# Kernel optimization log

Hardware: AMD Instinct MI355X
Metric: run time of the kernel (lower is better)

Reference implementation:

```python
import jax, jax.numpy as jnp
import numpy as np

N = 20000      # num_nodes
E = 320000     # num_edges
T = 24         # seq_len
SD = 16        # static_dim
DD = 8         # dynamic_dim
HID = 128      # hidden_dim
HEADS = 4
DPH = HID // HEADS  # per-head dim (GATConv out_channels = hidden_dim // heads)
L = 3          # num_gnn_layers
LN_EPS = 1e-5


def setup_inputs() -> dict:
    key = jax.random.key(0)
    ks = jax.random.split(key, 16)
    f = lambda i, shape, s=0.1: jax.random.normal(ks[i], shape, jnp.float32) * s
    return {
        "x_static": f(0, (N, SD), 1.0),
        "x_dynamic": f(1, (T, N, DD), 1.0),
        "edge_index": jax.random.randint(ks[2], (2, E), 0, N),
        "proj_W": f(3, (SD + DD, HID)),
        "proj_b": jnp.zeros((HID,), jnp.float32),
        "gat_W": f(4, (L, HID, HID)),
        "att_src": f(5, (L, HEADS, DPH)),
        "att_dst": f(6, (L, HEADS, DPH)),
        "gat_b": jnp.zeros((L, HID), jnp.float32),
        "ln_g": jnp.ones((L, HID), jnp.float32),
        "ln_b": jnp.zeros((L, HID), jnp.float32),
        "lstm_Wih0": f(7, (4 * HID, HID)),
        "lstm_Whh0": f(8, (4 * HID, HID)),
        "lstm_bih0": jnp.zeros((4 * HID,), jnp.float32),
        "lstm_bhh0": jnp.zeros((4 * HID,), jnp.float32),
        "lstm_Wih1": f(9, (4 * HID, HID)),
        "lstm_Whh1": f(10, (4 * HID, HID)),
        "lstm_bih1": jnp.zeros((4 * HID,), jnp.float32),
        "lstm_bhh1": jnp.zeros((4 * HID,), jnp.float32),
        "out_W1": f(11, (HID, HID // 2)),
        "out_b1": jnp.zeros((HID // 2,), jnp.float32),
        "out_W2": f(12, (HID // 2, 1)),
        "out_b2": jnp.zeros((1,), jnp.float32),
    }


def _gat_layer(h, src, dst, W, a_s, a_d, b, g, beta):
    """PyG GATConv (self-loops already in src/dst) + residual + LayerNorm + ReLU."""
    Nn = h.shape[0]
    xp = (h @ W).reshape(Nn, HEADS, DPH)                # [N, H, D]
    a_src = (xp * a_s).sum(-1)                          # [N, H]
    a_dst = (xp * a_d).sum(-1)                          # [N, H]
    e = jax.nn.leaky_relu(a_src[src] + a_dst[dst], 0.2)  # [E', H]
    m = jax.ops.segment_max(e, dst, num_segments=Nn)
    ex = jnp.exp(e - m[dst])
    denom = jax.ops.segment_sum(ex, dst, num_segments=Nn)
    alpha = ex / (denom[dst] + 1e-16)                   # segment softmax over in-edges
    msg = xp[src] * alpha[:, :, None]                   # [E', H, D]
    out = jax.ops.segment_sum(msg, dst, num_segments=Nn).reshape(Nn, HID) + b
    out = out + h                                       # residual (dims match)
    mu = out.mean(-1, keepdims=True)
    var = ((out - mu) ** 2).mean(-1, keepdims=True)
    out = g * (out - mu) * jax.lax.rsqrt(var + LN_EPS) + beta
    return jax.nn.relu(out)


def _lstm_cell(x, h, c, Wih, Whh, bih, bhh):
    z = x @ Wih.T + h @ Whh.T + bih + bhh
    i, f, gg, o = jnp.split(z, 4, axis=-1)              # torch gate order i,f,g,o
    c = jax.nn.sigmoid(f) * c + jax.nn.sigmoid(i) * jnp.tanh(gg)
    h = jax.nn.sigmoid(o) * jnp.tanh(c)
    return h, c


def reference(x_static, x_dynamic, edge_index, proj_W, proj_b, gat_W, att_src,
              att_dst, gat_b, ln_g, ln_b, lstm_Wih0, lstm_Whh0, lstm_bih0,
              lstm_bhh0, lstm_Wih1, lstm_Whh1, lstm_bih1, lstm_bhh1,
              out_W1, out_b1, out_W2, out_b2):
    Nn = x_static.shape[0]
    loop = jnp.arange(Nn)
    src = jnp.concatenate([edge_index[0], loop])        # GATConv add_self_loops=True
    dst = jnp.concatenate([edge_index[1], loop])

    @jax.checkpoint
    def timestep(xd_t):
        h = jnp.concatenate([x_static, xd_t], axis=-1) @ proj_W + proj_b
        for l in range(L):
            h = _gat_layer(h, src, dst, gat_W[l], att_src[l], att_dst[l],
                           gat_b[l], ln_g[l], ln_b[l])
        return h

    h_seq = jax.lax.map(timestep, x_dynamic)            # [T, N, HID]

    def step(carry, x_t):
        h0, c0, h1, c1 = carry
        h0, c0 = _lstm_cell(x_t, h0, c0, lstm_Wih0, lstm_Whh0, lstm_bih0, lstm_bhh0)
        h1, c1 = _lstm_cell(h0, h1, c1, lstm_Wih1, lstm_Whh1, lstm_bih1, lstm_bhh1)
        return (h0, c0, h1, c1), None

    z = jnp.zeros((Nn, HID), x_static.dtype)
    (_, _, h1, _), _ = jax.lax.scan(step, (z, z, z, z), h_seq)
    pred = jax.nn.relu(h1 @ out_W1 + out_b1) @ out_W2 + out_b2
    return pred[:, 0]
```

## Files before the change

kernel.cpp:

```cpp
#include <hip/hip_runtime.h>
#include <hip/hip_bf16.h>
#include <math.h>

#define NN   20000
#define NE   320000
#define TT   24
#define SDIM 16
#define DDIM 8
#define HID  128
#define HEADS 4
#define DPH  32
#define NL   3
#define TC   4

typedef unsigned short u16;
typedef unsigned int   u32;
typedef __attribute__((ext_vector_type(8))) short  short8;
typedef __attribute__((ext_vector_type(4))) float  floatx4;

__device__ __forceinline__ u16 f2bf(float x) {
  u32 u = __float_as_uint(x);
  return (u16)((u + 0x7fff + ((u >> 16) & 1)) >> 16);
}
__device__ __forceinline__ float bf2f(u16 b) {
  return __uint_as_float(((u32)b) << 16);
}

__global__ void k_count(const int* __restrict__ dst, int* __restrict__ cnt) {
  int e = blockIdx.x * 256 + threadIdx.x;
  if (e < NE) atomicAdd(&cnt[dst[e]], 1);
}

__global__ __launch_bounds__(1024) void k_scan(const int* __restrict__ cnt,
    int* __restrict__ rowptr, int* __restrict__ cursor) {
  __shared__ int sh[1024];
  int tid = threadIdx.x;
  const int CH = 20;
  int base = tid * CH;
  int local[CH];
  int s = 0;
  #pragma unroll
  for (int i = 0; i < CH; i++) {
    int idx = base + i;
    int v = (idx < NN) ? cnt[idx] : 0;
    local[i] = s;
    s += v;
  }
  sh[tid] = s;
  __syncthreads();
  for (int off = 1; off < 1024; off <<= 1) {
    int tv = (tid >= off) ? sh[tid - off] : 0;
    __syncthreads();
    sh[tid] += tv;
    __syncthreads();
  }
  int pre = (tid > 0) ? sh[tid - 1] : 0;
  #pragma unroll
  for (int i = 0; i < CH; i++) {
    int idx = base + i;
    if (idx < NN) { int e = pre + local[i]; rowptr[idx] = e; cursor[idx] = e; }
  }
  if (tid == 1023) rowptr[NN] = sh[1023];
}

__global__ void k_fill(const int* __restrict__ src, const int* __restrict__ dst,
    int* __restrict__ cursor, int* __restrict__ col, int* __restrict__ row) {
  int e = blockIdx.x * 256 + threadIdx.x;
  if (e < NE) {
    int d = dst[e];
    int pos = atomicAdd(&cursor[d], 1);
    col[pos] = src[e];
    row[pos] = d;
  }
}

__global__ void k_prepw_lstm(const float* __restrict__ Wih, const float* __restrict__ Whh,
    u16* __restrict__ Bt) {
  int idx = blockIdx.x * 256 + threadIdx.x;
  if (idx < 512 * 256) {
    int jp = idx >> 8, k = idx & 255;
    int c = jp >> 2, g = jp & 3;
    int j = g * 128 + c;
    float v = (k < 128) ? Wih[(size_t)j * 128 + k] : Whh[(size_t)j * 128 + (k - 128)];
    Bt[idx] = f2bf(v);
  }
}
__global__ void k_prepb(const float* __restrict__ bih0, const float* __restrict__ bhh0,
    const float* __restrict__ bih1, const float* __restrict__ bhh1,
    float* __restrict__ bs01) {
  int t = threadIdx.x;
  const float* bih = blockIdx.x ? bih1 : bih0;
  const float* bhh = blockIdx.x ? bhh1 : bhh0;
  int c = t >> 2, g = t & 3;
  bs01[blockIdx.x * 512 + t] = bih[g * 128 + c] + bhh[g * 128 + c];
}
__global__ void k_prepw_gat(const float* __restrict__ gatW, u16* __restrict__ Btg) {
  int idx = blockIdx.x * 256 + threadIdx.x;
  if (idx < NL * 128 * 128) {
    int l = idx >> 14, r = idx & 16383;
    int n = r >> 7, k = r & 127;
    Btg[idx] = f2bf(gatW[(size_t)l * 16384 + k * 128 + n]);
  }
}

__global__ __launch_bounds__(256) void k_proj(const float* __restrict__ xs,
    const float* __restrict__ xdt, const float* __restrict__ W,
    const float* __restrict__ b, u16* __restrict__ hbf) {
  __shared__ float Ws[24 * HID];
  __shared__ float xin[16][24];
  int tid = threadIdx.x;
  int tc = blockIdx.y;
  for (int i = tid; i < 24 * HID; i += 256) Ws[i] = W[i];
  int n0 = blockIdx.x * 16;
  for (int i = tid; i < 16 * 24; i += 256) {
    int r = i / 24, c = i % 24;
    int n = n0 + r;
    xin[r][c] = (c < SDIM) ? xs[(size_t)n * SDIM + c]
                           : xdt[(size_t)tc * NN * DDIM + (size_t)n * DDIM + (c - SDIM)];
  }
  __syncthreads();
  int ch = tid & 127, rb = (tid >> 7) * 8;
  for (int r = rb; r < rb + 8; r++) {
    float acc = b[ch];
    #pragma unroll
    for (int k = 0; k < 24; k++) acc = fmaf(xin[r][k], Ws[k * HID + ch], acc);
    hbf[((size_t)tc * NN + n0 + r) * HID + ch] = f2bf(acc);
  }
}

#define TBM 128
#define TBN 64
#define TBK 64

__global__ __launch_bounds__(256) void k_bgemm_gat(const u16* __restrict__ A,
    const u16* __restrict__ Bt, const float* __restrict__ as_,
    const float* __restrict__ ad_, u16* __restrict__ xpbf,
    float* __restrict__ asrc, float* __restrict__ adst, int M) {
  __shared__ u16 As[TBM][TBK + 8];
  __shared__ u16 Bs[TBN][TBK + 8];
  int tid = threadIdx.x;
  int wid = tid >> 6, lane = tid & 63;
  int wr = wid >> 1, wc = wid & 1;
  int lrow = lane & 15, lgrp = lane >> 4;
  int row0 = blockIdx.x * TBM, col0 = blockIdx.y * TBN;
  floatx4 acc[4][2] = {};
  for (int k0 = 0; k0 < 128; k0 += TBK) {
    #pragma unroll
    for (int i = 0; i < 4; i++) {
      int idx = tid + i * 256;
      int r = idx >> 3, g = idx & 7;
      int gr = row0 + r;
      short8 v = {};
      if (gr < M) v = *(const short8*)(A + (size_t)gr * 128 + k0 + g * 8);
      *(short8*)&As[r][g * 8] = v;
    }
    #pragma unroll
    for (int i = 0; i < 2; i++) {
      int idx = tid + i * 256;
      int r = idx >> 3, g = idx & 7;
      *(short8*)&Bs[r][g * 8] = *(const short8*)(Bt + (size_t)(col0 + r) * 128 + k0 + g * 8);
    }
    __syncthreads();
    #pragma unroll
    for (int kk = 0; kk < TBK; kk += 32) {
      short8 bfr[2];
      #pragma unroll
      for (int n = 0; n < 2; n++)
        bfr[n] = *(const short8*)&Bs[wc * 32 + n * 16 + lrow][kk + lgrp * 8];
      #pragma unroll
      for (int m = 0; m < 4; m++) {
        short8 af = *(const short8*)&As[wr * 64 + m * 16 + lrow][kk + lgrp * 8];
        acc[m][0] = __builtin_amdgcn_mfma_f32_16x16x32_bf16(af, bfr[0], acc[m][0], 0, 0, 0);
        acc[m][1] = __builtin_amdgcn_mfma_f32_16x16x32_bf16(af, bfr[1], acc[m][1], 0, 0, 0);
      }
    }
    __syncthreads();
  }
  int head = (col0 >> 5) + wc;
  float as0 = as_[head * 32 + lrow], as1 = as_[head * 32 + 16 + lrow];
  float ad0 = ad_[head * 32 + lrow], ad1 = ad_[head * 32 + 16 + lrow];
  #pragma unroll
  for (int m = 0; m < 4; m++) {
    #pragma unroll
    for (int r = 0; r < 4; r++) {
      int grow = row0 + wr * 64 + m * 16 + lgrp * 4 + r;
      float v0 = acc[m][0][r], v1 = acc[m][1][r];
      if (grow < M) {
        xpbf[(size_t)grow * HID + col0 + wc * 32 + lrow]      = f2bf(v0);
        xpbf[(size_t)grow * HID + col0 + wc * 32 + 16 + lrow] = f2bf(v1);
      }
      float ps = v0 * as0 + v1 * as1;
      float pd = v0 * ad0 + v1 * ad1;
      #pragma unroll
      for (int off = 1; off < 16; off <<= 1) {
        ps += __shfl_xor(ps, off);
        pd += __shfl_xor(pd, off);
      }
      if (lrow == 0 && grow < M) {
        asrc[grow * HEADS + head] = ps;
        adst[grow * HEADS + head] = pd;
      }
    }
  }
}

__global__ __launch_bounds__(256) void k_edgew(const int* __restrict__ col,
    const int* __restrict__ row, const float* __restrict__ asrc,
    const float* __restrict__ adst, float* __restrict__ wbuf) {
  int idx = blockIdx.x * 256 + threadIdx.x;
  int h = idx & 3;
  int je = idx >> 2;
  int tc = je / NE;
  int j = je - tc * NE;
  int base = tc * NN;
  float ev = asrc[(size_t)(base + col[j]) * HEADS + h]
           + adst[(size_t)(base + row[j]) * HEADS + h];
  ev = (ev > 0.f) ? ev : 0.2f * ev;
  wbuf[idx] = __expf(fminf(ev, 80.f));
}

__global__ __launch_bounds__(256) void k_aggr(const u16* __restrict__ xpbf,
    u16* __restrict__ hbf, const float* __restrict__ asrc,
    const float* __restrict__ adst, const float* __restrict__ wbuf,
    const int* __restrict__ rowptr, const int* __restrict__ col,
    const float* __restrict__ bias, const float* __restrict__ lng,
    const float* __restrict__ lnb) {
  int wid = threadIdx.x >> 6, lane = threadIdx.x & 63;
  int n = blockIdx.x * 4 + wid;
  int tc = n / NN;
  int node = n - tc * NN, base = tc * NN;
  int hh = lane >> 4;
  float ad = adst[n * HEADS + hh];
  float e0 = asrc[n * HEADS + hh] + ad;
  e0 = (e0 > 0.f) ? e0 : 0.2f * e0;
  float w0 = __expf(fminf(e0, 80.f));
  u32 xv = ((const u32*)(xpbf + (size_t)n * HID))[lane];
  float den0 = w0, den1 = 0.f, den2 = 0.f, den3 = 0.f;
  float p00 = w0 * bf2f((u16)(xv & 0xffff)), p10 = 0.f, p20 = 0.f, p30 = 0.f;
  float p01 = w0 * bf2f((u16)(xv >> 16)),    p11 = 0.f, p21 = 0.f, p31 = 0.f;
  const float* wrow = wbuf + (size_t)tc * NE * HEADS;
  int rs = rowptr[node], re = rowptr[node + 1];
  int j = rs;
  for (; j + 4 <= re; j += 4) {
    float w0e = wrow[(size_t)(j + 0) * HEADS + hh];
    float w1e = wrow[(size_t)(j + 1) * HEADS + hh];
    float w2e = wrow[(size_t)(j + 2) * HEADS + hh];
    float w3e = wrow[(size_t)(j + 3) * HEADS + hh];
    int s0 = base + col[j],     s1 = base + col[j + 1];
    int s2 = base + col[j + 2], s3 = base + col[j + 3];
    u32 x0 = ((const u32*)(xpbf + (size_t)s0 * HID))[lane];
    u32 x1 = ((const u32*)(xpbf + (size_t)s1 * HID))[lane];
    u32 x2 = ((const u32*)(xpbf + (size_t)s2 * HID))[lane];
    u32 x3 = ((const u32*)(xpbf + (size_t)s3 * HID))[lane];
    den0 += w0e; den1 += w1e; den2 += w2e; den3 += w3e;
    p00 = fmaf(w0e, bf2f((u16)(x0 & 0xffff)), p00);
    p10 = fmaf(w1e, bf2f((u16)(x1 & 0xffff)), p10);
    p20 = fmaf(w2e, bf2f((u16)(x2 & 0xffff)), p20);
    p30 = fmaf(w3e, bf2f((u16)(x3 & 0xffff)), p30);
    p01 = fmaf(w0e, bf2f((u16)(x0 >> 16)), p01);
    p11 = fmaf(w1e, bf2f((u16)(x1 >> 16)), p11);
    p21 = fmaf(w2e, bf2f((u16)(x2 >> 16)), p21);
    p31 = fmaf(w3e, bf2f((u16)(x3 >> 16)), p31);
  }
  for (; j < re; j++) {
    float w = wrow[(size_t)j * HEADS + hh];
    int s0 = base + col[j];
    u32 x0 = ((const u32*)(xpbf + (size_t)s0 * HID))[lane];
    den0 += w;
    p00 = fmaf(w, bf2f((u16)(x0 & 0xffff)), p00);
    p01 = fmaf(w, bf2f((u16)(x0 >> 16)), p01);
  }
  float den = (den0 + den1) + (den2 + den3);
  float mg0 = (p00 + p10) + (p20 + p30);
  float mg1 = (p01 + p11) + (p21 + p31);
  float inv = 1.f / (den + 1e-16f);
  int c0 = lane * 2;
  size_t hoff = (size_t)n * HID + c0;
  u32 hv = *(const u32*)(hbf + hoff);
  float o0 = mg0 * inv + bias[c0]     + bf2f((u16)(hv & 0xffff));
  float o1 = mg1 * inv + bias[c0 + 1] + bf2f((u16)(hv >> 16));
  float s2 = o0 + o1;
  #pragma unroll
  for (int off = 32; off; off >>= 1) s2 += __shfl_xor(s2, off);
  float mu = s2 * (1.f / HID);
  float d0 = o0 - mu, d1 = o1 - mu;
  float v2 = d0 * d0 + d1 * d1;
  #pragma unroll
  for (int off = 32; off; off >>= 1) v2 += __shfl_xor(v2, off);
  float rstd = rsqrtf(v2 * (1.f / HID) + 1e-5f);
  o0 = lng[c0] * d0 * rstd + lnb[c0];
  o1 = lng[c0 + 1] * d1 * rstd + lnb[c0 + 1];
  o0 = fmaxf(o0, 0.f);
  o1 = fmaxf(o1, 0.f);
  *(u32*)(hbf + hoff) = (u32)f2bf(o0) | ((u32)f2bf(o1) << 16);
}

__device__ __forceinline__ void lstm_body(const u16* __restrict__ A0,
    const u16* __restrict__ A1, const u16* __restrict__ Bt,
    const float* __restrict__ bs, float* __restrict__ cst,
    u16* __restrict__ hout, char* smem, int bx, int by) {
  u16 (*As)[TBK + 8] = (u16(*)[TBK + 8])smem;
  u16 (*Bs)[TBK + 8] = (u16(*)[TBK + 8])(smem + TBM * (TBK + 8) * 2);
  float (*zs)[68] = (float(*)[68])smem;
  int tid = threadIdx.x;
  int wid = tid >> 6, lane = tid & 63;
  int wr = wid >> 1, wc = wid & 1;
  int lrow = lane & 15, lgrp = lane >> 4;
  int row0 = bx * TBM, col0 = by * TBN;
  floatx4 acc[4][2] = {};
  for (int k0 = 0; k0 < 256; k0 += TBK) {
    const u16* Ap = (k0 < 128) ? A0 : A1;
    int kb = k0 & 127;
    #pragma unroll
    for (int i = 0; i < 4; i++) {
      int idx = tid + i * 256;
      int r = idx >> 3, g = idx & 7;
      int gr = row0 + r;
      short8 v = {};
      if (gr < NN) v = *(const short8*)(Ap + (size_t)gr * 128 + kb + g * 8);
      *(short8*)&As[r][g * 8] = v;
    }
    #pragma unroll
    for (int i = 0; i < 2; i++) {
      int idx = tid + i * 256;
      int r = idx >> 3, g = idx & 7;
      *(short8*)&Bs[r][g * 8] = *(const short8*)(Bt + (size_t)(col0 + r) * 256 + k0 + g * 8);
    }
    __syncthreads();
    #pragma unroll
    for (int kk = 0; kk < TBK; kk += 32) {
      short8 bfr[2];
      #pragma unroll
      for (int n = 0; n < 2; n++)
        bfr[n] = *(const short8*)&Bs[wc * 32 + n * 16 + lrow][kk + lgrp * 8];
      #pragma unroll
      for (int m = 0; m < 4; m++) {
        short8 af = *(const short8*)&As[wr * 64 + m * 16 + lrow][kk + lgrp * 8];
        acc[m][0] = __builtin_amdgcn_mfma_f32_16x16x32_bf16(af, bfr[0], acc[m][0], 0, 0, 0);
        acc[m][1] = __builtin_amdgcn_mfma_f32_16x16x32_bf16(af, bfr[1], acc[m][1], 0, 0, 0);
      }
    }
    __syncthreads();
  }
  #pragma unroll
  for (int m = 0; m < 4; m++)
    #pragma unroll
    for (int n = 0; n < 2; n++)
      #pragma unroll
      for (int r = 0; r < 4; r++)
        zs[wr * 64 + m * 16 + lgrp * 4 + r][wc * 32 + n * 16 + lrow] = acc[m][n][r];
  __syncthreads();
  int ch0 = by * 16;
  #pragma unroll
  for (int it = 0; it < 8; it++) {
    int o = tid + it * 256;
    int r = o >> 4, lc = o & 15;
    int grow = row0 + r;
    if (grow < NN) {
      float4 zi = *(float4*)&zs[r][lc * 4];
      int ch = ch0 + lc;
      size_t gi = (size_t)grow * HID + ch;
      float ii = zi.x + bs[4 * ch + 0];
      float ff = zi.y + bs[4 * ch + 1];
      float gg = zi.z + bs[4 * ch + 2];
      float oo = zi.w + bs[4 * ch + 3];
      float si = 1.f / (1.f + __expf(-ii));
      float sf = 1.f / (1.f + __expf(-ff));
      float so = 1.f / (1.f + __expf(-oo));
      float tg = tanhf(gg);
      float cn = sf * cst[gi] + si * tg;
      cst[gi] = cn;
      hout[gi] = f2bf(so * tanhf(cn));
    }
  }
}

__global__ __launch_bounds__(256) void k_lstm1(const u16* __restrict__ A0,
    const u16* __restrict__ A1, const u16* __restrict__ Bt,
    const float* __restrict__ bs, float* __restrict__ cst, u16* __restrict__ hout) {
  __shared__ __align__(16) char smem[34816];
  lstm_body(A0, A1, Bt, bs, cst, hout, smem, blockIdx.x, blockIdx.y);
}

__global__ __launch_bounds__(256) void k_lstm2(
    const u16* __restrict__ A0a, const u16* __restrict__ A1a, const u16* __restrict__ Bta,
    const float* __restrict__ bsa, float* __restrict__ csta, u16* __restrict__ houta,
    const u16* __restrict__ A0b, const u16* __restrict__ A1b, const u16* __restrict__ Btb,
    const float* __restrict__ bsb, float* __restrict__ cstb, u16* __restrict__ houtb) {
  __shared__ __align__(16) char smem[34816];
  if (blockIdx.z == 0) lstm_body(A0a, A1a, Bta, bsa, csta, houta, smem, blockIdx.x, blockIdx.y);
  else                 lstm_body(A0b, A1b, Btb, bsb, cstb, houtb, smem, blockIdx.x, blockIdx.y);
}

__global__ __launch_bounds__(64) void k_mlp(const u16* __restrict__ h1,
    const float* __restrict__ W1, const float* __restrict__ b1,
    const float* __restrict__ W2, const float* __restrict__ b2,
    float* __restrict__ out) {
  int n = blockIdx.x, j = threadIdx.x;
  const u16* hr = h1 + (size_t)n * HID;
  float acc = b1[j];
  #pragma unroll 8
  for (int k = 0; k < HID; k++) acc = fmaf(bf2f(hr[k]), W1[(size_t)k * 64 + j], acc);
  acc = fmaxf(acc, 0.f);
  float p = acc * W2[j];
  #pragma unroll
  for (int off = 32; off; off >>= 1) p += __shfl_xor(p, off);
  if (j == 0) out[n] = p + b2[0];
}

extern "C" void kernel_launch(void* const* d_in, const int* in_sizes, int n_in,
                              void* d_out, int out_size, void* d_ws, size_t ws_size,
                              hipStream_t stream) {
  const float* xs    = (const float*)d_in[0];
  const float* xd    = (const float*)d_in[1];
  const int*   ei    = (const int*)d_in[2];
  const float* projW = (const float*)d_in[3];
  const float* projb = (const float*)d_in[4];
  const float* gatW  = (const float*)d_in[5];
  const float* attS  = (const float*)d_in[6];
  const float* attD  = (const float*)d_in[7];
  const float* gatb  = (const float*)d_in[8];
  const float* lng   = (const float*)d_in[9];
  const float* lnb   = (const float*)d_in[10];
  const float* Wih0  = (const float*)d_in[11];
  const float* Whh0  = (const float*)d_in[12];
  const float* bih0  = (const float*)d_in[13];
  const float* bhh0  = (const float*)d_in[14];
  const float* Wih1  = (const float*)d_in[15];
  const float* Whh1  = (const float*)d_in[16];
  const float* bih1  = (const float*)d_in[17];
  const float* bhh1  = (const float*)d_in[18];
  const float* oW1   = (const float*)d_in[19];
  const float* ob1   = (const float*)d_in[20];
  const float* oW2   = (const float*)d_in[21];
  const float* ob2   = (const float*)d_in[22];
  float* out = (float*)d_out;

  char* w = (char*)d_ws;
  size_t off = 0;
  auto alloc = [&](size_t bytes) { void* p = w + off; off += (bytes + 255) & ~(size_t)255; return p; };
  u16*   hbf   = (u16*)  alloc((size_t)TC * NN * HID * 2);
  u16*   xpbf  = (u16*)  alloc((size_t)TC * NN * HID * 2);
  float* asrc  = (float*)alloc((size_t)TC * NN * HEADS * 4);
  float* adst  = (float*)alloc((size_t)TC * NN * HEADS * 4);
  float* wbuf  = (float*)alloc((size_t)TC * NE * HEADS * 4);
  float* c01   = (float*)alloc((size_t)2 * NN * HID * 4);
  float* c0 = c01, *c1 = c01 + (size_t)NN * HID;
  u16*   h0p   = (u16*)  alloc((size_t)2 * NN * HID * 2);
  u16*   h1p   = (u16*)  alloc((size_t)2 * NN * HID * 2);
  u16*   h0buf[2] = { h0p, h0p + (size_t)NN * HID };
  u16*   h1buf[2] = { h1p, h1p + (size_t)NN * HID };
  u16*   Wc0bf = (u16*)alloc((size_t)512 * 256 * 2);
  u16*   Wc1bf = (u16*)alloc((size_t)512 * 256 * 2);
  float* bs01  = (float*)alloc((size_t)1024 * 4);
  float* bs0 = bs01, *bs1 = bs01 + 512;
  u16*   gatWbf= (u16*)alloc((size_t)NL * 128 * 128 * 2);
  int* cnt    = (int*)alloc((size_t)NN * 4);
  int* rowptr = (int*)alloc((size_t)(NN + 1) * 4);
  int* cursor = (int*)alloc((size_t)NN * 4);
  int* col    = (int*)alloc((size_t)NE * 4);
  int* rowi   = (int*)alloc((size_t)NE * 4);

  const int* esrc = ei;
  const int* edst = ei + NE;

  hipMemsetAsync(cnt, 0, (size_t)NN * 4, stream);
  k_count<<<(NE + 255) / 256, 256, 0, stream>>>(edst, cnt);
  k_scan<<<1, 1024, 0, stream>>>(cnt, rowptr, cursor);
  k_fill<<<(NE + 255) / 256, 256, 0, stream>>>(esrc, edst, cursor, col, rowi);

  k_prepw_lstm<<<(512 * 256) / 256, 256, 0, stream>>>(Wih0, Whh0, Wc0bf);
  k_prepw_lstm<<<(512 * 256) / 256, 256, 0, stream>>>(Wih1, Whh1, Wc1bf);
  k_prepb<<<2, 512, 0, stream>>>(bih0, bhh0, bih1, bhh1, bs01);
  k_prepw_gat<<<(NL * 128 * 128) / 256, 256, 0, stream>>>(gatW, gatWbf);
  hipMemsetAsync(c01, 0, (size_t)2 * NN * HID * 4, stream);
  hipMemsetAsync(h0buf[0], 0, (size_t)NN * HID * 2, stream);
  hipMemsetAsync(h1buf[0], 0, (size_t)NN * HID * 2, stream);

  const int gx  = (NN + TBM - 1) / TBM;
  const int gx2 = (TC * NN + TBM - 1) / TBM;

  auto gnn_chunk = [&](int tcb) {
    k_proj<<<dim3(NN / 16, TC), 256, 0, stream>>>(
        xs, xd + (size_t)(tcb * TC) * NN * DDIM, projW, projb, hbf);
    for (int l = 0; l < NL; l++) {
      k_bgemm_gat<<<dim3(gx2, 2), 256, 0, stream>>>(
          hbf, gatWbf + (size_t)l * 128 * 128,
          attS + l * HEADS * DPH, attD + l * HEADS * DPH,
          xpbf, asrc, adst, TC * NN);
      k_edgew<<<(TC * NE * HEADS) / 256, 256, 0, stream>>>(col, rowi, asrc, adst, wbuf);
      k_aggr<<<TC * NN / 4, 256, 0, stream>>>(
          xpbf, hbf, asrc, adst, wbuf, rowptr, col, gatb + (size_t)l * HID,
          lng + (size_t)l * HID, lnb + (size_t)l * HID);
    }
  };
  auto lstm_merged = [&](int t) {
    int pi = t & 1;
    int s1 = (t + 1) & (TC - 1);
    k_lstm2<<<dim3(gx, 8, 2), 256, 0, stream>>>(
        h0buf[pi ^ 1], h1buf[pi], Wc1bf, bs1, c1, h1buf[pi ^ 1],
        hbf + (size_t)s1 * NN * HID, h0buf[pi ^ 1], Wc0bf, bs0, c0, h0buf[pi]);
  };

  gnn_chunk(0);
  k_lstm1<<<dim3(gx, 8), 256, 0, stream>>>(hbf, h0buf[0], Wc0bf, bs0, c0, h0buf[1]);
  lstm_merged(0); lstm_merged(1); lstm_merged(2);
  for (int tcb = 1; tcb < TT / TC; tcb++) {
    gnn_chunk(tcb);
    lstm_merged(4 * tcb - 1);
    lstm_merged(4 * tcb);
    lstm_merged(4 * tcb + 1);
    if (tcb < TT / TC - 1) lstm_merged(4 * tcb + 2);
    else {
      lstm_merged(4 * tcb + 2);
      k_lstm1<<<dim3(gx, 8), 256, 0, stream>>>(h0buf[0], h1buf[1], Wc1bf, bs1, c1, h1buf[0]);
    }
  }

  k_mlp<<<NN, 64, 0, stream>>>(h1buf[0], oW1, ob1, oW2, ob2, out);
}
```

Before: 3.318 ms.

## Batch timestep chunk per edge in GAT aggregation and drop LDS staging in LSTM epilogue

The edge-weight kernel now computes all four timesteps of a chunk per edge and packs them as bf16 into one 64-bit word. The aggregation kernel handles one node across all four timesteps, so each edge's column index and weights are loaded once and shared across the 16 lanes of a head by shuffles. This cuts index and weight traffic and shrinks the weight buffer, at the cost of bf16 precision on attention weights and more registers per thread. The LSTM epilogue now regroups the MFMA accumulators with lane shuffles instead of an LDS round trip and a barrier, which also shrinks shared memory.

```diff
diff --git a/kernel.cpp b/kernel.cpp
--- a/kernel.cpp
+++ b/kernel.cpp
@@ -15,6 +15,7 @@
 
 typedef unsigned short u16;
 typedef unsigned int   u32;
+typedef unsigned long long u64;
 typedef __attribute__((ext_vector_type(8))) short  short8;
 typedef __attribute__((ext_vector_type(4))) float  floatx4;
 
@@ -206,93 +207,93 @@
 
 __global__ __launch_bounds__(256) void k_edgew(const int* __restrict__ col,
     const int* __restrict__ row, const float* __restrict__ asrc,
-    const float* __restrict__ adst, float* __restrict__ wbuf) {
+    const float* __restrict__ adst, u64* __restrict__ ewq) {
   int idx = blockIdx.x * 256 + threadIdx.x;
-  int h = idx & 3;
-  int je = idx >> 2;
-  int tc = je / NE;
-  int j = je - tc * NE;
-  int base = tc * NN;
-  float ev = asrc[(size_t)(base + col[j]) * HEADS + h]
-           + adst[(size_t)(base + row[j]) * HEADS + h];
-  ev = (ev > 0.f) ? ev : 0.2f * ev;
-  wbuf[idx] = __expf(fminf(ev, 80.f));
+  int j = idx >> 2, h = idx & 3;
+  int c = col[j], r = row[j];
+  u64 w = 0;
+  #pragma unroll
+  for (int tc = 0; tc < TC; tc++) {
+    float ev = asrc[((size_t)tc * NN + c) * HEADS + h]
+             + adst[((size_t)tc * NN + r) * HEADS + h];
+    ev = (ev > 0.f) ? ev : 0.2f * ev;
+    w |= ((u64)f2bf(__expf(fminf(ev, 80.f)))) << (tc * 16);
+  }
+  ewq[idx] = w;
 }
 
 __global__ __launch_bounds__(256) void k_aggr(const u16* __restrict__ xpbf,
     u16* __restrict__ hbf, const float* __restrict__ asrc,
-    const float* __restrict__ adst, const float* __restrict__ wbuf,
+    const float* __restrict__ adst, const u64* __restrict__ ewq,
     const int* __restrict__ rowptr, const int* __restrict__ col,
     const float* __restrict__ bias, const float* __restrict__ lng,
     const float* __restrict__ lnb) {
   int wid = threadIdx.x >> 6, lane = threadIdx.x & 63;
-  int n = blockIdx.x * 4 + wid;
-  int tc = n / NN;
-  int node = n - tc * NN, base = tc * NN;
-  int hh = lane >> 4;
-  float ad = adst[n * HEADS + hh];
-  float e0 = asrc[n * HEADS + hh] + ad;
-  e0 = (e0 > 0.f) ? e0 : 0.2f * e0;
-  float w0 = __expf(fminf(e0, 80.f));
-  u32 xv = ((const u32*)(xpbf + (size_t)n * HID))[lane];
-  float den0 = w0, den1 = 0.f, den2 = 0.f, den3 = 0.f;
-  float p00 = w0 * bf2f((u16)(xv & 0xffff)), p10 = 0.f, p20 = 0.f, p30 = 0.f;
-  float p01 = w0 * bf2f((u16)(xv >> 16)),    p11 = 0.f, p21 = 0.f, p31 = 0.f;
-  const float* wrow = wbuf + (size_t)tc * NE * HEADS;
+  int node = blockIdx.x * 4 + wid;
+  int hh = lane >> 4, lrow = lane & 15;
+  int c0 = lane * 2;
+  float bi0 = bias[c0], bi1 = bias[c0 + 1];
+  float g0 = lng[c0], g1 = lng[c0 + 1];
+  float lb0 = lnb[c0], lb1 = lnb[c0 + 1];
+  float den[TC], p0[TC], p1[TC];
+  u32 hv[TC];
+  #pragma unroll
+  for (int tc = 0; tc < TC; tc++) {
+    size_t n = (size_t)tc * NN + node;
+    float ad = adst[n * HEADS + hh];
+    float e0 = asrc[n * HEADS + hh] + ad;
+    e0 = (e0 > 0.f) ? e0 : 0.2f * e0;
+    float w0 = __expf(fminf(e0, 80.f));
+    u32 xv = ((const u32*)(xpbf + n * HID))[lane];
+    den[tc] = w0;
+    p0[tc] = w0 * bf2f((u16)(xv & 0xffff));
+    p1[tc] = w0 * bf2f((u16)(xv >> 16));
+    hv[tc] = *(const u32*)(hbf + n * HID + c0);
+  }
   int rs = rowptr[node], re = rowptr[node + 1];
-  int j = rs;
-  for (; j + 4 <= re; j += 4) {
-    float w0e = wrow[(size_t)(j + 0) * HEADS + hh];
-    float w1e = wrow[(size_t)(j + 1) * HEADS + hh];
-    float w2e = wrow[(size_t)(j + 2) * HEADS + hh];
-    float w3e = wrow[(size_t)(j + 3) * HEADS + hh];
-    int s0 = base + col[j],     s1 = base + col[j + 1];
-    int s2 = base + col[j + 2], s3 = base + col[j + 3];
-    u32 x0 = ((const u32*)(xpbf + (size_t)s0 * HID))[lane];
-    u32 x1 = ((const u32*)(xpbf + (size_t)s1 * HID))[lane];
-    u32 x2 = ((const u32*)(xpbf + (size_t)s2 * HID))[lane];
-    u32 x3 = ((const u32*)(xpbf + (size_t)s3 * HID))[lane];
-    den0 += w0e; den1 += w1e; den2 += w2e; den3 += w3e;
-    p00 = fmaf(w0e, bf2f((u16)(x0 & 0xffff)), p00);
-    p10 = fmaf(w1e, bf2f((u16)(x1 & 0xffff)), p10);
-    p20 = fmaf(w2e, bf2f((u16)(x2 & 0xffff)), p20);
-    p30 = fmaf(w3e, bf2f((u16)(x3 & 0xffff)), p30);
-    p01 = fmaf(w0e, bf2f((u16)(x0 >> 16)), p01);
-    p11 = fmaf(w1e, bf2f((u16)(x1 >> 16)), p11);
-    p21 = fmaf(w2e, bf2f((u16)(x2 >> 16)), p21);
-    p31 = fmaf(w3e, bf2f((u16)(x3 >> 16)), p31);
-  }
-  for (; j < re; j++) {
-    float w = wrow[(size_t)j * HEADS + hh];
-    int s0 = base + col[j];
-    u32 x0 = ((const u32*)(xpbf + (size_t)s0 * HID))[lane];
-    den0 += w;
-    p00 = fmaf(w, bf2f((u16)(x0 & 0xffff)), p00);
-    p01 = fmaf(w, bf2f((u16)(x0 >> 16)), p01);
-  }
-  float den = (den0 + den1) + (den2 + den3);
-  float mg0 = (p00 + p10) + (p20 + p30);
-  float mg1 = (p01 + p11) + (p21 + p31);
-  float inv = 1.f / (den + 1e-16f);
-  int c0 = lane * 2;
-  size_t hoff = (size_t)n * HID + c0;
-  u32 hv = *(const u32*)(hbf + hoff);
-  float o0 = mg0 * inv + bias[c0]     + bf2f((u16)(hv & 0xffff));
-  float o1 = mg1 * inv + bias[c0 + 1] + bf2f((u16)(hv >> 16));
-  float s2 = o0 + o1;
-  #pragma unroll
-  for (int off = 32; off; off >>= 1) s2 += __shfl_xor(s2, off);
-  float mu = s2 * (1.f / HID);
-  float d0 = o0 - mu, d1 = o1 - mu;
-  float v2 = d0 * d0 + d1 * d1;
-  #pragma unroll
-  for (int off = 32; off; off >>= 1) v2 += __shfl_xor(v2, off);
-  float rstd = rsqrtf(v2 * (1.f / HID) + 1e-5f);
-  o0 = lng[c0] * d0 * rstd + lnb[c0];
-  o1 = lng[c0 + 1] * d1 * rstd + lnb[c0 + 1];
-  o0 = fmaxf(o0, 0.f);
-  o1 = fmaxf(o1, 0.f);
-  *(u32*)(hbf + hoff) = (u32)f2bf(o0) | ((u32)f2bf(o1) << 16);
+  for (int tile = rs; tile < re; tile += 16) {
+    int cnt = re - tile; if (cnt > 16) cnt = 16;
+    int e = tile + lrow;
+    int cl = 0; u32 wlo = 0, whi = 0;
+    if (e < re) {
+      cl = col[e];
+      u64 wq = ewq[(size_t)e * HEADS + hh];
+      wlo = (u32)wq; whi = (u32)(wq >> 32);
+    }
+    for (int k = 0; k < cnt; k++) {
+      int sk = __shfl(cl, k, 16);
+      u32 wl = (u32)__shfl((int)wlo, k, 16);
+      u32 wh = (u32)__shfl((int)whi, k, 16);
+      float w_[TC] = { bf2f((u16)(wl & 0xffff)), bf2f((u16)(wl >> 16)),
+                       bf2f((u16)(wh & 0xffff)), bf2f((u16)(wh >> 16)) };
+      #pragma unroll
+      for (int tc = 0; tc < TC; tc++) {
+        u32 x = ((const u32*)(xpbf + ((size_t)tc * NN + sk) * HID))[lane];
+        den[tc] += w_[tc];
+        p0[tc] = fmaf(w_[tc], bf2f((u16)(x & 0xffff)), p0[tc]);
+        p1[tc] = fmaf(w_[tc], bf2f((u16)(x >> 16)), p1[tc]);
+      }
+    }
+  }
+  #pragma unroll
+  for (int tc = 0; tc < TC; tc++) {
+    size_t hoff = ((size_t)tc * NN + node) * HID + c0;
+    float inv = 1.f / (den[tc] + 1e-16f);
+    float o0 = p0[tc] * inv + bi0 + bf2f((u16)(hv[tc] & 0xffff));
+    float o1 = p1[tc] * inv + bi1 + bf2f((u16)(hv[tc] >> 16));
+    float s2 = o0 + o1;
+    #pragma unroll
+    for (int off = 32; off; off >>= 1) s2 += __shfl_xor(s2, off);
+    float mu = s2 * (1.f / HID);
+    float d0 = o0 - mu, d1 = o1 - mu;
+    float v2 = d0 * d0 + d1 * d1;
+    #pragma unroll
+    for (int off = 32; off; off >>= 1) v2 += __shfl_xor(v2, off);
+    float rstd = rsqrtf(v2 * (1.f / HID) + 1e-5f);
+    o0 = fmaxf(g0 * d0 * rstd + lb0, 0.f);
+    o1 = fmaxf(g1 * d1 * rstd + lb1, 0.f);
+    *(u32*)(hbf + hoff) = (u32)f2bf(o0) | ((u32)f2bf(o1) << 16);
+  }
 }
 
 __device__ __forceinline__ void lstm_body(const u16* __restrict__ A0,
@@ -301,7 +302,6 @@
     u16* __restrict__ hout, char* smem, int bx, int by) {
   u16 (*As)[TBK + 8] = (u16(*)[TBK + 8])smem;
   u16 (*Bs)[TBK + 8] = (u16(*)[TBK + 8])(smem + TBM * (TBK + 8) * 2);
-  float (*zs)[68] = (float(*)[68])smem;
   int tid = threadIdx.x;
   int wid = tid >> 6, lane = tid & 63;
   int wr = wid >> 1, wc = wid & 1;
@@ -342,35 +342,47 @@
     }
     __syncthreads();
   }
-  #pragma unroll
-  for (int m = 0; m < 4; m++)
-    #pragma unroll
-    for (int n = 0; n < 2; n++)
-      #pragma unroll
-      for (int r = 0; r < 4; r++)
-        zs[wr * 64 + m * 16 + lgrp * 4 + r][wc * 32 + n * 16 + lrow] = acc[m][n][r];
-  __syncthreads();
-  int ch0 = by * 16;
-  #pragma unroll
-  for (int it = 0; it < 8; it++) {
-    int o = tid + it * 256;
-    int r = o >> 4, lc = o & 15;
-    int grow = row0 + r;
-    if (grow < NN) {
-      float4 zi = *(float4*)&zs[r][lc * 4];
-      int ch = ch0 + lc;
-      size_t gi = (size_t)grow * HID + ch;
-      float ii = zi.x + bs[4 * ch + 0];
-      float ff = zi.y + bs[4 * ch + 1];
-      float gg = zi.z + bs[4 * ch + 2];
-      float oo = zi.w + bs[4 * ch + 3];
-      float si = 1.f / (1.f + __expf(-ii));
-      float sf = 1.f / (1.f + __expf(-ff));
-      float so = 1.f / (1.f + __expf(-oo));
-      float tg = tanhf(gg);
-      float cn = sf * cst[gi] + si * tg;
-      cst[gi] = cn;
-      hout[gi] = f2bf(so * tanhf(cn));
+  int q = lrow >> 2, s = lrow & 3;
+  bool odd_s = (lane & 1), hi_s = (lane & 2);
+  int ch[2]; float4 bsv[2];
+  #pragma unroll
+  for (int n = 0; n < 2; n++) {
+    ch[n] = by * 16 + wc * 8 + n * 4 + q;
+    bsv[n] = *(const float4*)&bs[4 * ch[n]];
+  }
+  #pragma unroll
+  for (int m = 0; m < 4; m++) {
+    int grow = row0 + wr * 64 + m * 16 + lgrp * 4 + s;
+    bool ok = grow < NN;
+    #pragma unroll
+    for (int n = 0; n < 2; n++) {
+      float a0 = acc[m][n][0], a1 = acc[m][n][1], a2 = acc[m][n][2], a3 = acc[m][n][3];
+      float e0 = __shfl_xor(a1, 1), e1 = __shfl_xor(a0, 1);
+      float e2 = __shfl_xor(a3, 1), e3 = __shfl_xor(a2, 1);
+      float t0 = odd_s ? e0 : a0;
+      float t1 = odd_s ? a1 : e1;
+      float t2 = odd_s ? e2 : a2;
+      float t3 = odd_s ? a3 : e3;
+      float f0 = __shfl_xor(t2, 2), f2 = __shfl_xor(t0, 2);
+      float f1 = __shfl_xor(t3, 2), f3 = __shfl_xor(t1, 2);
+      float b0 = hi_s ? f0 : t0;
+      float b1 = hi_s ? f1 : t1;
+      float b2 = hi_s ? t2 : f2;
+      float b3 = hi_s ? t3 : f3;
+      if (ok) {
+        size_t gi = (size_t)grow * HID + ch[n];
+        float ii = b0 + bsv[n].x;
+        float ff = b1 + bsv[n].y;
+        float gg = b2 + bsv[n].z;
+        float oo = b3 + bsv[n].w;
+        float si = 1.f / (1.f + __expf(-ii));
+        float sf = 1.f / (1.f + __expf(-ff));
+        float so = 1.f / (1.f + __expf(-oo));
+        float tg = tanhf(gg);
+        float cn = sf * cst[gi] + si * tg;
+        cst[gi] = cn;
+        hout[gi] = f2bf(so * tanhf(cn));
+      }
     }
   }
 }
@@ -378,7 +390,7 @@
 __global__ __launch_bounds__(256) void k_lstm1(const u16* __restrict__ A0,
     const u16* __restrict__ A1, const u16* __restrict__ Bt,
     const float* __restrict__ bs, float* __restrict__ cst, u16* __restrict__ hout) {
-  __shared__ __align__(16) char smem[34816];
+  __shared__ __align__(16) char smem[27648];
   lstm_body(A0, A1, Bt, bs, cst, hout, smem, blockIdx.x, blockIdx.y);
 }
 
@@ -387,7 +399,7 @@
     const float* __restrict__ bsa, float* __restrict__ csta, u16* __restrict__ houta,
     const u16* __restrict__ A0b, const u16* __restrict__ A1b, const u16* __restrict__ Btb,
     const float* __restrict__ bsb, float* __restrict__ cstb, u16* __restrict__ houtb) {
-  __shared__ __align__(16) char smem[34816];
+  __shared__ __align__(16) char smem[27648];
   if (blockIdx.z == 0) lstm_body(A0a, A1a, Bta, bsa, csta, houta, smem, blockIdx.x, blockIdx.y);
   else                 lstm_body(A0b, A1b, Btb, bsb, cstb, houtb, smem, blockIdx.x, blockIdx.y);
 }
@@ -443,7 +455,7 @@
   u16*   xpbf  = (u16*)  alloc((size_t)TC * NN * HID * 2);
   float* asrc  = (float*)alloc((size_t)TC * NN * HEADS * 4);
   float* adst  = (float*)alloc((size_t)TC * NN * HEADS * 4);
-  float* wbuf  = (float*)alloc((size_t)TC * NE * HEADS * 4);
+  u64*   ewq   = (u64*)  alloc((size_t)NE * HEADS * 8);
   float* c01   = (float*)alloc((size_t)2 * NN * HID * 4);
   float* c0 = c01, *c1 = c01 + (size_t)NN * HID;
   u16*   h0p   = (u16*)  alloc((size_t)2 * NN * HID * 2);
@@ -488,9 +500,9 @@
           hbf, gatWbf + (size_t)l * 128 * 128,
           attS + l * HEADS * DPH, attD + l * HEADS * DPH,
           xpbf, asrc, adst, TC * NN);
-      k_edgew<<<(TC * NE * HEADS) / 256, 256, 0, stream>>>(col, rowi, asrc, adst, wbuf);
-      k_aggr<<<TC * NN / 4, 256, 0, stream>>>(
-          xpbf, hbf, asrc, adst, wbuf, rowptr, col, gatb + (size_t)l * HID,
+      k_edgew<<<(NE * HEADS) / 256, 256, 0, stream>>>(col, rowi, asrc, adst, ewq);
+      k_aggr<<<NN / 4, 256, 0, stream>>>(
+          xpbf, hbf, asrc, adst, ewq, rowptr, col, gatb + (size_t)l * HID,
           lng + (size_t)l * HID, lnb + (size_t)l * HID);
     }
   };
```

Measured after the change: 3.288 ms. Within noise of the previous version (-0.9%).
